# Performance work log

Measured on AMD Instinct MI355X. Metric: run time of the kernel, lower is better.

The kernel has to match this reference:

```python
import jax, jax.numpy as jnp
import numpy as np

B = 32          # graphs per batch
NPG = 512       # nodes per graph
EPG = 2048      # original edges per graph (stored in y[:, -1])
N = B * NPG     # 16384 nodes
E = B * EPG     # 65536 edges
GF = 5          # num_global_features
ETOT = E + N    # edges after add_self_loops

def _lin(k, o, i):
    return jax.random.normal(k, (o, i), jnp.float32) / np.sqrt(i)

def setup_inputs():
    key = jax.random.key(0)
    ks = jax.random.split(key, 20)
    x = jax.random.normal(ks[0], (N,), jnp.float32)
    off = (jnp.arange(B, dtype=jnp.int32) * NPG)[:, None]
    src = (jax.random.randint(ks[1], (B, EPG), 0, NPG, dtype=jnp.int32) + off).reshape(-1)
    dst = (jax.random.randint(ks[2], (B, EPG), 0, NPG, dtype=jnp.int32) + off).reshape(-1)
    edge_index = jnp.stack([src, dst])
    edge_attr = jax.random.normal(ks[3], (E, GF), jnp.float32)
    # last global feature = number of edges per graph (module reads y[:, -1])
    y = jax.random.normal(ks[4], (B, GF), jnp.float32).at[:, -1].set(float(EPG)).reshape(-1)
    batch_vector = jnp.repeat(jnp.arange(B, dtype=jnp.int32), NPG)
    p = dict(
        Wn=_lin(ks[5], 512, 1), bn=jnp.zeros(512, jnp.float32),
        We=_lin(ks[6], 511, GF), be=jnp.zeros(511, jnp.float32),
        Wg=_lin(ks[7], 512, GF), bg=jnp.zeros(512, jnp.float32),
        Wl=_lin(ks[8], 1024, 512), bl=jnp.zeros(1024, jnp.float32),
        Wr=_lin(ks[9], 1024, 512), br=jnp.zeros(1024, jnp.float32),
        Wge=_lin(ks[10], 1024, 511),
        att=jax.random.normal(ks[11], (1024,), jnp.float32) / 32.0,
        bgat=jnp.zeros(1024, jnp.float32),
        Wm=_lin(ks[12], 1024, 1024), bm=jnp.zeros(1024, jnp.float32),
        Wmi=_lin(ks[13], 1024, 1024), bmi=jnp.zeros(1024, jnp.float32),
        Wce=_lin(ks[14], 1024, 512), bce=jnp.zeros(1024, jnp.float32),
        W1=_lin(ks[15], 256, 2048), b1=jnp.zeros(256, jnp.float32),
        W2=_lin(ks[16], 1, 256), b2=jnp.zeros(1, jnp.float32),
    )
    return dict(x=x, edge_index=edge_index, edge_attr=edge_attr, y=y,
                batch_vector=batch_vector, **p)

def _leaky(v, s=0.01):
    return jnp.where(v >= 0, v, s * v)

def _forward(edge_index, batch_vector, x, edge_attr, y, Wn, bn, We, be, Wg, bg,
             Wl, bl, Wr, br, Wge, att, bgat, Wm, bm, Wmi, bmi, Wce, bce,
             W1, b1, W2, b2):
    # add_self_loops (fill_value=1.0 for edge_attr), self loops appended last
    loops = jnp.arange(N, dtype=edge_index.dtype)
    src = jnp.concatenate([edge_index[0], loops])
    dst = jnp.concatenate([edge_index[1], loops])
    ea = jnp.concatenate([edge_attr, jnp.ones((N, GF), edge_attr.dtype)], axis=0)
    # preprocessing MLPs (dropout = identity at inference)
    h = _leaky(x[:, None] @ Wn.T + bn)               # [N, 512]
    e = _leaky(ea @ We.T + be)                       # [ETOT, 511]
    yg = _leaky(y.reshape(B, GF) @ Wg.T + bg)        # [B, 512]
    # GATv2Conv, 1 head, concat, negative_slope=0.2, no self-loop add
    xl = h @ Wl.T + bl                               # source transform [N, 1024]
    xr = h @ Wr.T + br                               # target transform [N, 1024]
    m = _leaky(xl[src] + xr[dst] + e @ Wge.T, 0.2)   # [ETOT, 1024]
    logit = m @ att                                  # [ETOT]
    mx = jax.ops.segment_max(logit, dst, num_segments=N)
    ex = jnp.exp(logit - mx[dst])
    alpha = ex / (jax.ops.segment_sum(ex, dst, num_segments=N)[dst] + 1e-16)
    gat = jax.ops.segment_sum(alpha[:, None] * xl[src], dst, num_segments=N) + bgat
    edge_total = jnp.concatenate([e, alpha[:, None]], axis=1)  # [ETOT, 512]
    # GeneralConv: undirected message, add aggregation, identity skip (in==out)
    hm = gat @ Wm.T + bm
    hmi = gat @ Wmi.T + bmi
    eh = edge_total @ Wce.T + bce                    # [ETOT, 1024]
    deg = jax.ops.segment_sum(jnp.ones((ETOT,), gat.dtype), dst, num_segments=N)
    conv = (jax.ops.segment_sum(hm[src] + eh, dst, num_segments=N)
            + deg[:, None] * hmi + gat)              # [N, 1024]
    # global mean pooling (nodes) and module's contiguous edge batch vector
    nc = jax.ops.segment_sum(jnp.ones((N,), conv.dtype), batch_vector, num_segments=B)
    pn = jax.ops.segment_sum(conv, batch_vector, num_segments=B) / nc[:, None]
    ebatch = jnp.repeat(jnp.arange(B, dtype=jnp.int32), EPG + NPG)
    pe = jax.ops.segment_sum(edge_total, ebatch, num_segments=B) / float(EPG + NPG)
    pooled = jnp.concatenate([pn, pe, yg], axis=1)   # [B, 2048]
    out = _leaky(pooled @ W1.T + b1) @ W2.T + b2
    return jax.nn.sigmoid(out)                       # [B, 1]

def reference(x, edge_index, edge_attr, y, batch_vector, Wn, bn, We, be, Wg, bg,
              Wl, bl, Wr, br, Wge, att, bgat, Wm, bm, Wmi, bmi, Wce, bce,
              W1, b1, W2, b2):
    return _forward(edge_index, batch_vector, x, edge_attr, y, Wn, bn, We, be,
                    Wg, bg, Wl, bl, Wr, br, Wge, att, bgat, Wm, bm, Wmi, bmi,
                    Wce, bce, W1, b1, W2, b2)
```

## Files before the change

### kernel.cpp

```cpp
#include <hip/hip_runtime.h>
#include <cstdint>
#include <cstddef>

#define N_NODES 16384
#define N_EDGES 65536
#define ETOT    81920
#define B_GR    32

typedef __attribute__((ext_vector_type(8))) short bf16x8;
typedef __attribute__((ext_vector_type(4))) float f32x4;

static constexpr size_t OFF_XL    = 0;
static constexpr size_t OFF_XR    = 33554432ULL;
static constexpr size_t OFF_EBF   = 67108864ULL;
static constexpr size_t OFF_HBF   = 67108864ULL;
static constexpr size_t OFF_WCAT  = 83886080ULL;
static constexpr size_t OFF_ROWP  = 67108864ULL;
static constexpr size_t OFF_CSR   = 67174656ULL;
static constexpr size_t OFF_ALPHA = 67502336ULL;
static constexpr size_t OFF_WGEP  = 134217728ULL;
static constexpr size_t OFF_LPART = 135266304ULL;
static constexpr size_t OFF_DEG   = 137363456ULL;
static constexpr size_t OFF_ODEG  = 137428992ULL;
static constexpr size_t OFF_CURS  = 137494528ULL;
static constexpr size_t OFF_PG    = 137560064ULL;
static constexpr size_t OFF_PDG   = 137691136ULL;
static constexpr size_t OFF_PGAT  = 137822208ULL;
static constexpr size_t OFF_PS    = 137953280ULL;
static constexpr size_t OFF_PE    = 138018816ULL;
static constexpr size_t OFF_WLOOP = 138084352ULL;
static constexpr size_t OFF_YG    = 138088448ULL;
static constexpr size_t OFF_PN    = 138153984ULL;
static constexpr size_t OFF_OPRE  = 138285056ULL;

__device__ __forceinline__ float leaky01(float v){ return v >= 0.f ? v : 0.01f*v; }
__device__ __forceinline__ float leaky02(float v){ return v >= 0.f ? v : 0.2f*v; }
__device__ __forceinline__ unsigned short f2bf(float f){
  union { float f; unsigned u; } v; v.f = f;
  unsigned r = v.u + 0x7FFFu + ((v.u >> 16) & 1u);
  return (unsigned short)(r >> 16);
}
__device__ __forceinline__ float bf2f(unsigned short h){
  union { unsigned u; float f; } v; v.u = ((unsigned)h) << 16;
  return v.f;
}

__global__ __launch_bounds__(256) void k_prep0(
    const float* __restrict__ x, const float* __restrict__ Wn, const float* __restrict__ bn,
    const float* __restrict__ Wl, const float* __restrict__ Wr,
    const float* __restrict__ Wge, const float* __restrict__ y,
    const float* __restrict__ Wg, const float* __restrict__ bg,
    const float* __restrict__ We, const float* __restrict__ be,
    float* __restrict__ zone, unsigned short* __restrict__ h_bf,
    unsigned short* __restrict__ Wcat, unsigned short* __restrict__ Wge_p,
    float* __restrict__ yg, float* __restrict__ we_loop) {
  __shared__ float e_lds[512];
  int bx = blockIdx.x, tid = threadIdx.x;
  if (bx < 176) {
    ((float4*)zone)[bx*256 + tid] = (float4){0.f,0.f,0.f,0.f};
  } else if (bx < 1200) {
    int gid = (bx-176)*256 + tid;
    int base = gid*8;
    int n = base >> 9, j = base & 511;
    float xv = x[n];
    float4 w0 = *(const float4*)(Wn + j);
    float4 w1 = *(const float4*)(Wn + j + 4);
    float4 b0 = *(const float4*)(bn + j);
    float4 b1 = *(const float4*)(bn + j + 4);
    unsigned short o[8];
    o[0]=f2bf(leaky01(xv*w0.x+b0.x)); o[1]=f2bf(leaky01(xv*w0.y+b0.y));
    o[2]=f2bf(leaky01(xv*w0.z+b0.z)); o[3]=f2bf(leaky01(xv*w0.w+b0.w));
    o[4]=f2bf(leaky01(xv*w1.x+b1.x)); o[5]=f2bf(leaky01(xv*w1.y+b1.y));
    o[6]=f2bf(leaky01(xv*w1.z+b1.z)); o[7]=f2bf(leaky01(xv*w1.w+b1.w));
    ((uint4*)h_bf)[gid] = *(const uint4*)o;
  } else if (bx < 2224) {
    int i = (bx-1200)*256 + tid;
    int base = i*4;
    const float* src = (base < 524288) ? (Wl + base) : (Wr + base - 524288);
    float4 v = *(const float4*)src;
    ushort4 o; o.x=f2bf(v.x); o.y=f2bf(v.y); o.z=f2bf(v.z); o.w=f2bf(v.w);
    ((ushort4*)Wcat)[i] = o;
  } else if (bx < 4272) {
    int gid = (bx-2224)*256 + tid;
    int j = gid >> 9, k = gid & 511;
    Wge_p[gid] = (k < 511) ? f2bf(Wge[(size_t)j*511 + k]) : (unsigned short)0;
  } else if (bx < 4336) {
    int gid = (bx-4272)*256 + tid;
    int b = gid >> 9, j = gid & 511;
    float s = bg[j];
    #pragma unroll
    for (int k=0;k<5;k++) s += y[b*5+k]*Wg[j*5+k];
    yg[gid] = leaky01(s);
  } else {
    for (int c = tid; c < 512; c += 256) {
      float v = 0.f;
      if (c < 511) {
        float s = be[c];
        #pragma unroll
        for (int q=0;q<5;q++) s += We[c*5+q];
        v = leaky01(s);
      }
      e_lds[c] = v;
    }
    __syncthreads();
    int j = (bx-4336)*256 + tid;
    float s = 0.f;
    for (int k=0;k<511;k++) s += e_lds[k]*Wge[(size_t)j*511+k];
    we_loop[j] = s;
  }
}

__global__ __launch_bounds__(256) void k_prep_e(
    const float* __restrict__ ea, const float* __restrict__ We, const float* __restrict__ be,
    unsigned short* __restrict__ E_bf,
    const int* __restrict__ ei, int* __restrict__ deg, int* __restrict__ odeg) {
  int blk = blockIdx.x;
  if (blk < 16384) {
    int gid = blk*256 + threadIdx.x;
    int e = gid >> 6, cg = gid & 63;
    int c0 = cg*8;
    const float* e5 = ea + (size_t)e*5;
    float a0=e5[0], a1=e5[1], a2=e5[2], a3=e5[3], a4=e5[4];
    unsigned short o[8];
    #pragma unroll
    for (int j=0;j<8;j++) {
      int c = c0 + j;
      float v = 0.f;
      if (c < 511) {
        const float* w = We + c*5;
        float s = be[c] + a0*w[0] + a1*w[1] + a2*w[2] + a3*w[3] + a4*w[4];
        v = leaky01(s);
      }
      o[j] = f2bf(v);
    }
    ((uint4*)E_bf)[gid] = *(const uint4*)o;
  } else {
    int i = (blk-16384)*256 + threadIdx.x;
    int s, d;
    if (i < N_EDGES) { s = ei[i]; d = ei[N_EDGES + i]; }
    else { s = i - N_EDGES; d = s; }
    atomicAdd(&deg[d], 1);
    atomicAdd(&odeg[s], 1);
  }
}

__global__ __launch_bounds__(1024) void k_scan(const int* __restrict__ deg, int* __restrict__ rowptr) {
  __shared__ int sums[1024];
  int t = threadIdx.x;
  int local[16]; int s = 0;
  #pragma unroll
  for (int i=0;i<16;i++){ local[i] = deg[t*16+i]; s += local[i]; }
  sums[t] = s; __syncthreads();
  for (int off=1; off<1024; off<<=1) {
    int v = (t >= off) ? sums[t-off] : 0;
    __syncthreads();
    sums[t] += v;
    __syncthreads();
  }
  int run = (t==0) ? 0 : sums[t-1];
  if (t==0) rowptr[0] = 0;
  #pragma unroll
  for (int i=0;i<16;i++){ run += local[i]; rowptr[t*16+i+1] = run; }
}

__global__ void k_fill_csr(const int* __restrict__ ei, const int* __restrict__ rowptr,
                           int* __restrict__ cursor, int* __restrict__ csr) {
  int i = blockIdx.x*blockDim.x + threadIdx.x;
  int d = (i < N_EDGES) ? ei[N_EDGES + i] : (i - N_EDGES);
  int pos = rowptr[d] + atomicAdd(&cursor[d], 1);
  csr[pos] = i;
}


__global__ __launch_bounds__(256) void k_gemm_xlxr(
    const unsigned short* __restrict__ h_bf, const unsigned short* __restrict__ Wcat,
    const float* __restrict__ bl, const float* __restrict__ br,
    unsigned short* __restrict__ xl_bf, unsigned short* __restrict__ xr_bf) {
  __shared__ unsigned short As[2][4096];
  __shared__ unsigned short Bs[2][4096];
  int blk = blockIdx.x;
  int xcd = blk & 7, slot = blk >> 3;
  int bx = xcd*16 + (slot >> 4), by = slot & 15;
  int row0 = bx*128, col0 = by*128;
  int tid = threadIdx.x;
  int w = tid >> 6, lane = tid & 63;
  int wm = w >> 1, wn = w & 1;
  int quad = lane >> 4, l16 = lane & 15;
  int ldoff = w*512 + lane*8;
  const unsigned short* gA = h_bf + (size_t)(row0 + w*16 + l16)*512 + quad*8;
  const unsigned short* gB = Wcat + (size_t)(col0 + w*16 + l16)*512 + quad*8;
  f32x4 acc[4][4];
  #pragma unroll
  for (int i=0;i<4;i++)
    #pragma unroll
    for (int j=0;j<4;j++) acc[i][j] = (f32x4){0.f,0.f,0.f,0.f};

  {
    uint4 a0 = *(const uint4*)(gA);
    uint4 a1 = *(const uint4*)(gA + 32768);
    uint4 b0 = *(const uint4*)(gB);
    uint4 b1 = *(const uint4*)(gB + 32768);
    *(uint4*)&As[0][ldoff] = a0; *(uint4*)&As[0][2048+ldoff] = a1;
    *(uint4*)&Bs[0][ldoff] = b0; *(uint4*)&Bs[0][2048+ldoff] = b1;
  }
  __syncthreads();
  int cur = 0;
  #pragma unroll 2
  for (int k0 = 32; k0 <= 512; k0 += 32) {
    uint4 na0, na1, nb0, nb1;
    bool more = (k0 < 512);
    if (more) {
      na0 = *(const uint4*)(gA + k0);
      na1 = *(const uint4*)(gA + 32768 + k0);
      nb0 = *(const uint4*)(gB + k0);
      nb1 = *(const uint4*)(gB + 32768 + k0);
    }
    bf16x8 af[4], bfr[4];
    #pragma unroll
    for (int mi=0;mi<4;mi++)
      af[mi] = *(const bf16x8*)&As[cur][(wm*4+mi)*512 + quad*128 + l16*8];
    #pragma unroll
    for (int ni=0;ni<4;ni++)
      bfr[ni] = *(const bf16x8*)&Bs[cur][(wn*4+ni)*512 + quad*128 + l16*8];
    #pragma unroll
    for (int mi=0;mi<4;mi++)
      #pragma unroll
      for (int ni=0;ni<4;ni++)
        acc[mi][ni] = __builtin_amdgcn_mfma_f32_16x16x32_bf16(af[mi], bfr[ni], acc[mi][ni], 0, 0, 0);
    if (more) {
      *(uint4*)&As[cur^1][ldoff] = na0; *(uint4*)&As[cur^1][2048+ldoff] = na1;
      *(uint4*)&Bs[cur^1][ldoff] = nb0; *(uint4*)&Bs[cur^1][2048+ldoff] = nb1;
    }
    __syncthreads();
    cur ^= 1;
  }
  bool isL = (by < 8);
  const float* bias = isL ? bl : br;
  unsigned short* O = isL ? xl_bf : xr_bf;
  int cb = isL ? col0 : (col0 - 1024);
  float bias4[4];
  #pragma unroll
  for (int ni=0;ni<4;ni++) bias4[ni] = bias[cb + wn*64 + ni*16 + l16];
  #pragma unroll
  for (int mi=0;mi<4;mi++)
    #pragma unroll
    for (int ni=0;ni<4;ni++) {
      int col = cb + wn*64 + ni*16 + l16;
      #pragma unroll
      for (int r=0;r<4;r++) {
        int row = row0 + wm*64 + mi*16 + quad*4 + r;
        O[(size_t)row*1024 + col] = f2bf(acc[mi][ni][r] + bias4[ni]);
      }
    }
}

__global__ __launch_bounds__(256) void k_mfma_we(
    const unsigned short* __restrict__ E_bf, const unsigned short* __restrict__ Wge_bf,
    const int* __restrict__ ei,
    const unsigned short* __restrict__ xl_bf, const unsigned short* __restrict__ xr_bf,
    const float* __restrict__ att, float* __restrict__ logit_part) {
  __shared__ unsigned short As[2][4096];
  __shared__ unsigned short Bs[2][4096];
  __shared__ float tmp[128];
  int blk = blockIdx.x;
  int xcd = blk & 7, slot = blk >> 3;
  int bx = xcd*64 + (slot >> 3), by = slot & 7;
  int row0 = bx*128, col0 = by*128;
  int tid = threadIdx.x;
  int w = tid >> 6, lane = tid & 63;
  int wm = w >> 1, wn = w & 1;
  int quad = lane >> 4, l16 = lane & 15;
  int ldoff = w*512 + lane*8;
  const unsigned short* gA = E_bf  + (size_t)(row0 + w*16 + l16)*512 + quad*8;
  const unsigned short* gB = Wge_bf + (size_t)(col0 + w*16 + l16)*512 + quad*8;
  f32x4 acc[4][4];
  #pragma unroll
  for (int i=0;i<4;i++)
    #pragma unroll
    for (int j=0;j<4;j++) acc[i][j] = (f32x4){0.f,0.f,0.f,0.f};

  {
    uint4 a0 = *(const uint4*)(gA);
    uint4 a1 = *(const uint4*)(gA + 32768);
    uint4 b0 = *(const uint4*)(gB);
    uint4 b1 = *(const uint4*)(gB + 32768);
    *(uint4*)&As[0][ldoff] = a0; *(uint4*)&As[0][2048+ldoff] = a1;
    *(uint4*)&Bs[0][ldoff] = b0; *(uint4*)&Bs[0][2048+ldoff] = b1;
  }
  __syncthreads();
  int cur = 0;
  #pragma unroll 2
  for (int k0 = 32; k0 <= 512; k0 += 32) {
    uint4 na0, na1, nb0, nb1;
    bool more = (k0 < 512);
    if (more) {
      na0 = *(const uint4*)(gA + k0);
      na1 = *(const uint4*)(gA + 32768 + k0);
      nb0 = *(const uint4*)(gB + k0);
      nb1 = *(const uint4*)(gB + 32768 + k0);
    }
    bf16x8 af[4], bfr[4];
    #pragma unroll
    for (int mi=0;mi<4;mi++)
      af[mi] = *(const bf16x8*)&As[cur][(wm*4+mi)*512 + quad*128 + l16*8];
    #pragma unroll
    for (int ni=0;ni<4;ni++)
      bfr[ni] = *(const bf16x8*)&Bs[cur][(wn*4+ni)*512 + quad*128 + l16*8];
    #pragma unroll
    for (int mi=0;mi<4;mi++)
      #pragma unroll
      for (int ni=0;ni<4;ni++)
        acc[mi][ni] = __builtin_amdgcn_mfma_f32_16x16x32_bf16(af[mi], bfr[ni], acc[mi][ni], 0, 0, 0);
    if (more) {
      *(uint4*)&As[cur^1][ldoff] = na0; *(uint4*)&As[cur^1][2048+ldoff] = na1;
      *(uint4*)&Bs[cur^1][ldoff] = nb0; *(uint4*)&Bs[cur^1][2048+ldoff] = nb1;
    }
    __syncthreads();
    cur ^= 1;
  }
  float att4[4];
  #pragma unroll
  for (int ni=0;ni<4;ni++) att4[ni] = att[col0 + wn*64 + ni*16 + l16];
  float pv[4][4];
  #pragma unroll
  for (int mi=0;mi<4;mi++) {
    #pragma unroll
    for (int r=0;r<4;r++) {
      int e = row0 + wm*64 + mi*16 + quad*4 + r;
      int s = ei[e], d = ei[N_EDGES + e];
      const unsigned short* xlr = xl_bf + (size_t)s*1024;
      const unsigned short* xrr = xr_bf + (size_t)d*1024;
      float p = 0.f;
      #pragma unroll
      for (int ni=0;ni<4;ni++) {
        int col = col0 + wn*64 + ni*16 + l16;
        float z = acc[mi][ni][r] + bf2f(xlr[col]) + bf2f(xrr[col]);
        z = leaky02(z);
        p += z*att4[ni];
      }
      p += __shfl_down(p, 8, 16);
      p += __shfl_down(p, 4, 16);
      p += __shfl_down(p, 2, 16);
      p += __shfl_down(p, 1, 16);
      pv[mi][r] = p;
    }
  }
  if (wn == 1 && l16 == 0) {
    #pragma unroll
    for (int mi=0;mi<4;mi++)
      #pragma unroll
      for (int r=0;r<4;r++)
        tmp[wm*64 + mi*16 + quad*4 + r] = pv[mi][r];
  }
  __syncthreads();
  if (wn == 0 && l16 == 0) {
    #pragma unroll
    for (int mi=0;mi<4;mi++)
      #pragma unroll
      for (int r=0;r<4;r++) {
        int le = wm*64 + mi*16 + quad*4 + r;
        logit_part[(size_t)(row0 + le)*8 + by] = pv[mi][r] + tmp[le];
      }
  }
}

__global__ __launch_bounds__(256) void k_softmax_gat(
    const int* __restrict__ ei, const int* __restrict__ rowptr, const int* __restrict__ csr,
    const float* __restrict__ logit_part,
    const unsigned short* __restrict__ xl_bf, const unsigned short* __restrict__ xr_bf,
    const float* __restrict__ we_loop, const float* __restrict__ att,
    const float* __restrict__ bgat,
    float* __restrict__ alpha, unsigned short* __restrict__ gat_bf) {
  int blk = blockIdx.x;
  int wid = threadIdx.x >> 6, lane = threadIdx.x & 63;
  int n = ((blk & 7) << 11) + ((blk >> 3) << 2) + wid;
  int c0 = lane*16;

  float sll;
  {
    const uint4* xp = (const uint4*)(xl_bf + (size_t)n*1024 + c0);
    const uint4* rp = (const uint4*)(xr_bf + (size_t)n*1024 + c0);
    uint4 xa0 = xp[0], xa1 = xp[1];
    uint4 xb0 = rp[0], xb1 = rp[1];
    const unsigned short* ua = (const unsigned short*)&xa0;
    const unsigned short* ub = (const unsigned short*)&xb0;
    const unsigned short* ua1 = (const unsigned short*)&xa1;
    const unsigned short* ub1 = (const unsigned short*)&xb1;
    float s = 0.f;
    #pragma unroll
    for (int j=0;j<8;j++) {
      float z = bf2f(ua[j]) + bf2f(ub[j]) + we_loop[c0+j];
      s += leaky02(z) * att[c0+j];
    }
    #pragma unroll
    for (int j=0;j<8;j++) {
      float z = bf2f(ua1[j]) + bf2f(ub1[j]) + we_loop[c0+8+j];
      s += leaky02(z) * att[c0+8+j];
    }
    #pragma unroll
    for (int m=1; m<64; m<<=1) s += __shfl_xor(s, m);
    sll = s;
  }

  int beg = rowptr[n], end = rowptr[n+1];
  int cnt = end - beg;

  float acc[16];
  {
    const float4* bp = (const float4*)(bgat + c0);
    float4 b0 = bp[0], b1 = bp[1], b2 = bp[2], b3 = bp[3];
    acc[0]=b0.x; acc[1]=b0.y; acc[2]=b0.z; acc[3]=b0.w;
    acc[4]=b1.x; acc[5]=b1.y; acc[6]=b1.z; acc[7]=b1.w;
    acc[8]=b2.x; acc[9]=b2.y; acc[10]=b2.z; acc[11]=b2.w;
    acc[12]=b3.x; acc[13]=b3.y; acc[14]=b3.z; acc[15]=b3.w;
  }

  if (cnt <= 64) {
    int p = beg + lane;
    bool act = (p < end);
    int e = 0, src = 0;
    float lg = -1e30f;
    if (act) {
      e = csr[p];
      if (e < N_EDGES) {
        const float4* lp = (const float4*)(logit_part + (size_t)e*8);
        float4 q0 = lp[0], q1 = lp[1];
        lg = q0.x+q0.y+q0.z+q0.w+q1.x+q1.y+q1.z+q1.w;
        src = ei[e];
      } else { lg = sll; src = e - N_EDGES; }
    }
    float mx = lg;
    #pragma unroll
    for (int m=1; m<64; m<<=1) mx = fmaxf(mx, __shfl_xor(mx, m));
    float ex = act ? expf(lg - mx) : 0.f;
    float ss = ex;
    #pragma unroll
    for (int m=1; m<64; m<<=1) ss += __shfl_xor(ss, m);
    float a = ex * (1.f/(ss + 1e-16f));
    if (act) alpha[e] = a;
    for (int q = 0; q < cnt; q++) {
      float aq = __shfl(a, q);
      int sq = __shfl(src, q);
      const uint4* xp = (const uint4*)(xl_bf + (size_t)sq*1024 + c0);
      uint4 u0 = xp[0], u1 = xp[1];
      const unsigned short* uu0 = (const unsigned short*)&u0;
      const unsigned short* uu1 = (const unsigned short*)&u1;
      #pragma unroll
      for (int j=0;j<8;j++) acc[j]   += aq * bf2f(uu0[j]);
      #pragma unroll
      for (int j=0;j<8;j++) acc[8+j] += aq * bf2f(uu1[j]);
    }
  } else {
    float mx = -1e30f;
    for (int p = beg + lane; p < end; p += 64) {
      int e = csr[p];
      float lg;
      if (e < N_EDGES) {
        const float4* lp = (const float4*)(logit_part + (size_t)e*8);
        float4 q0 = lp[0], q1 = lp[1];
        lg = q0.x+q0.y+q0.z+q0.w+q1.x+q1.y+q1.z+q1.w;
      } else lg = sll;
      mx = fmaxf(mx, lg);
    }
    #pragma unroll
    for (int m=1; m<64; m<<=1) mx = fmaxf(mx, __shfl_xor(mx, m));
    float ss = 0.f;
    for (int p = beg + lane; p < end; p += 64) {
      int e = csr[p];
      float lg;
      if (e < N_EDGES) {
        const float4* lp = (const float4*)(logit_part + (size_t)e*8);
        float4 q0 = lp[0], q1 = lp[1];
        lg = q0.x+q0.y+q0.z+q0.w+q1.x+q1.y+q1.z+q1.w;
      } else lg = sll;
      ss += expf(lg - mx);
    }
    #pragma unroll
    for (int m=1; m<64; m<<=1) ss += __shfl_xor(ss, m);
    float inv = 1.f/(ss + 1e-16f);

    for (int p0 = beg; p0 < end; p0 += 64) {
      int p = p0 + lane;
      float a = 0.f; int src = 0;
      if (p < end) {
        int e = csr[p];
        float lg;
        if (e < N_EDGES) {
          const float4* lp = (const float4*)(logit_part + (size_t)e*8);
          float4 q0 = lp[0], q1 = lp[1];
          lg = q0.x+q0.y+q0.z+q0.w+q1.x+q1.y+q1.z+q1.w;
          src = ei[e];
        } else { lg = sll; src = e - N_EDGES; }
        a = expf(lg - mx)*inv;
        alpha[e] = a;
      }
      int kmax = end - p0; if (kmax > 64) kmax = 64;
      for (int q = 0; q < kmax; q++) {
        float aq = __shfl(a, q);
        int sq = __shfl(src, q);
        const uint4* xp = (const uint4*)(xl_bf + (size_t)sq*1024 + c0);
        uint4 u0 = xp[0], u1 = xp[1];
        const unsigned short* uu0 = (const unsigned short*)&u0;
        const unsigned short* uu1 = (const unsigned short*)&u1;
        #pragma unroll
        for (int j=0;j<8;j++) acc[j]   += aq * bf2f(uu0[j]);
        #pragma unroll
        for (int j=0;j<8;j++) acc[8+j] += aq * bf2f(uu1[j]);
      }
    }
  }

  unsigned short o[16];
  #pragma unroll
  for (int j=0;j<16;j++) o[j] = f2bf(acc[j]);
  uint4* gp = (uint4*)(gat_bf + (size_t)n*1024 + c0);
  gp[0] = *(const uint4*)&o[0];
  gp[1] = *(const uint4*)&o[8];
}

__global__ __launch_bounds__(256) void k_pool(
    const unsigned short* __restrict__ gat_bf, const int* __restrict__ odeg,
    const int* __restrict__ rowptr,
    float* __restrict__ P_G, float* __restrict__ P_DG, float* __restrict__ P_gat,
    const float* __restrict__ ea, const float* __restrict__ We, const float* __restrict__ be,
    const float* __restrict__ alpha, float* __restrict__ P_S, float* __restrict__ pe) {
  __shared__ float sea[640];
  __shared__ float sal[128];
  int slot = blockIdx.x, tid = threadIdx.x;
  if (slot < 512) {
    int b = slot >> 4, nc = slot & 15;
    int c4 = tid;
    float a1[4]={0,0,0,0}, a2[4]={0,0,0,0}, a3[4]={0,0,0,0};
    int n0 = b*512 + nc*32;
    for (int i=0;i<32;i++){
      int n = n0 + i;
      ushort4 g4 = ((const ushort4*)(gat_bf + (size_t)n*1024))[c4];
      float od = (float)odeg[n];
      float dg = (float)(rowptr[n+1]-rowptr[n]);
      float g0 = bf2f(g4.x), g1 = bf2f(g4.y), g2 = bf2f(g4.z), g3 = bf2f(g4.w);
      a1[0]+=od*g0; a1[1]+=od*g1; a1[2]+=od*g2; a1[3]+=od*g3;
      a2[0]+=dg*g0; a2[1]+=dg*g1; a2[2]+=dg*g2; a2[3]+=dg*g3;
      a3[0]+=g0; a3[1]+=g1; a3[2]+=g2; a3[3]+=g3;
    }
    #pragma unroll
    for (int j=0;j<4;j++){
      atomicAdd(&P_G [b*1024 + c4*4+j], a1[j]);
      atomicAdd(&P_DG[b*1024 + c4*4+j], a2[j]);
      atomicAdd(&P_gat[b*1024 + c4*4+j], a3[j]);
    }
  } else {
    int s = slot - 512;
    int b = s & 31, chy = s >> 5;
    int mode = (chy < 20) ? 0 : 1;
    int ch = (chy < 20) ? chy : (chy - 20);
    int c1 = tid, c2 = tid + 256;
    bool v2 = (c2 < 511);
    float w1[5], w2[5]={0,0,0,0,0}, b1v, b2v=0.f;
    #pragma unroll
    for (int q=0;q<5;q++) w1[q] = We[c1*5+q];
    b1v = be[c1];
    if (v2) {
      #pragma unroll
      for (int q=0;q<5;q++) w2[q] = We[c2*5+q];
      b2v = be[c2];
    }
    int base = (mode == 0)
      ? ((ch < 16) ? (b*2048 + ch*128) : (N_EDGES + b*512 + (ch-16)*128))
      : (b*2560 + ch*128);
    for (int i=tid;i<640;i+=256){
      int r = base + i/5;
      sea[i] = (r < N_EDGES) ? ea[(size_t)r*5 + (i%5)] : 1.0f;
    }
    for (int i=tid;i<128;i+=256) sal[i] = alpha[base + i];
    __syncthreads();
    float acc1 = 0.f, acc2 = 0.f;
    for (int rr=0; rr<128; rr++) {
      const float* er = &sea[rr*5];
      acc1 += leaky01(b1v + er[0]*w1[0]+er[1]*w1[1]+er[2]*w1[2]+er[3]*w1[3]+er[4]*w1[4]);
      if (v2) acc2 += leaky01(b2v + er[0]*w2[0]+er[1]*w2[1]+er[2]*w2[2]+er[3]*w2[3]+er[4]*w2[4]);
      else    acc2 += sal[rr];
    }
    if (mode == 0) {
      atomicAdd(&P_S[b*512+c1], acc1);
      atomicAdd(&P_S[b*512+c2], acc2);
    } else {
      const float sc = 1.f/2560.f;
      atomicAdd(&pe[b*512+c1], acc1*sc);
      atomicAdd(&pe[b*512+c2], acc2*sc);
    }
  }
}

__global__ __launch_bounds__(256) void k_pn(
    const float* __restrict__ P_G, const float* __restrict__ P_DG,
    const float* __restrict__ P_S, const float* __restrict__ P_gat,
    const float* __restrict__ Wm, const float* __restrict__ bm,
    const float* __restrict__ Wmi, const float* __restrict__ bmi,
    const float* __restrict__ Wce, const float* __restrict__ bce,
    float* __restrict__ pn, float* __restrict__ out_pre) {
  __shared__ float sPg[1024], sPdg[1024], sPs[512];
  int blk = blockIdx.x;
  int xcd = blk & 7, slot = blk >> 3;
  int colgrp = xcd*2 + (slot & 1);
  int b = slot >> 1;
  int col0 = colgrp*64;
  int tid = threadIdx.x, w = tid >> 6, lane = tid & 63;
  if (blk == 0 && tid < 32) out_pre[tid] = 0.f;
  for (int i=tid;i<1024;i+=256){ sPg[i]=P_G[b*1024+i]; sPdg[i]=P_DG[b*1024+i]; }
  for (int i=tid;i<512;i+=256) sPs[i]=P_S[b*512+i];
  __syncthreads();
  for (int c=0;c<16;c++){
    int j = col0 + w*16 + c;
    const float* wm  = Wm  + (size_t)j*1024;
    const float* wmi = Wmi + (size_t)j*1024;
    const float* wce = Wce + (size_t)j*512;
    float s = 0.f;
    #pragma unroll 4
    for (int i=0;i<16;i++){ int k = lane + i*64; s += sPg[k]*wm[k] + sPdg[k]*wmi[k]; }
    #pragma unroll 4
    for (int i=0;i<8;i++){ int k = lane + i*64; s += sPs[k]*wce[k]; }
    #pragma unroll
    for (int off=32; off; off>>=1) s += __shfl_down(s, off);
    if (lane == 0) {
      pn[b*1024+j] = (s + P_gat[b*1024+j] + 2560.f*(bm[j]+bmi[j]+bce[j])) * (1.f/512.f);
    }
  }
}

__global__ __launch_bounds__(256) void k_final(
    const float* __restrict__ pn, const float* __restrict__ pe, const float* __restrict__ yg,
    const float* __restrict__ W1, const float* __restrict__ b1,
    const float* __restrict__ W2, float* __restrict__ out_pre) {
  __shared__ float pooled[2048];
  int blk = blockIdx.x;
  int hc = blk & 7, b = blk >> 3;
  int tid = threadIdx.x;
  for (int i=tid;i<1024;i+=256) pooled[i]      = pn[b*1024+i];
  for (int i=tid;i<512;i+=256)  pooled[1024+i] = pe[b*512+i];
  for (int i=tid;i<512;i+=256)  pooled[1536+i] = yg[b*512+i];
  __syncthreads();
  int r = hc*32 + (tid >> 3);
  int seg = tid & 7;
  const float4* w4 = (const float4*)(W1 + (size_t)r*2048 + seg*256);
  const float4* p4 = (const float4*)(pooled + seg*256);
  float s = 0.f;
  #pragma unroll 8
  for (int k=0;k<64;k++){
    float4 w = w4[k]; float4 p = p4[k];
    s += w.x*p.x + w.y*p.y + w.z*p.z + w.w*p.w;
  }
  s += __shfl_down(s, 4, 8);
  s += __shfl_down(s, 2, 8);
  s += __shfl_down(s, 1, 8);
  if (seg == 0) {
    float h = leaky01(s + b1[r]);
    atomicAdd(&out_pre[b], h * W2[r]);
  }
}

__global__ void k_sigmoid(const float* __restrict__ out_pre, const float* __restrict__ b2,
                          float* __restrict__ out) {
  int b = threadIdx.x;
  out[b] = 1.f/(1.f + expf(-(out_pre[b] + b2[0])));
}

extern "C" void kernel_launch(void* const* d_in, const int* in_sizes, int n_in,
                              void* d_out, int out_size, void* d_ws, size_t ws_size,
                              hipStream_t stream) {
  const float* x   = (const float*)d_in[0];
  const int*   ei  = (const int*)  d_in[1];
  const float* ea  = (const float*)d_in[2];
  const float* y   = (const float*)d_in[3];
  const float* Wn  = (const float*)d_in[5];
  const float* bn  = (const float*)d_in[6];
  const float* We  = (const float*)d_in[7];
  const float* be  = (const float*)d_in[8];
  const float* Wg  = (const float*)d_in[9];
  const float* bg  = (const float*)d_in[10];
  const float* Wl  = (const float*)d_in[11];
  const float* bl  = (const float*)d_in[12];
  const float* Wr  = (const float*)d_in[13];
  const float* br  = (const float*)d_in[14];
  const float* Wge = (const float*)d_in[15];
  const float* att = (const float*)d_in[16];
  const float* bgat= (const float*)d_in[17];
  const float* Wm  = (const float*)d_in[18];
  const float* bm  = (const float*)d_in[19];
  const float* Wmi = (const float*)d_in[20];
  const float* bmi = (const float*)d_in[21];
  const float* Wce = (const float*)d_in[22];
  const float* bce = (const float*)d_in[23];
  const float* W1  = (const float*)d_in[24];
  const float* b1  = (const float*)d_in[25];
  const float* W2  = (const float*)d_in[26];
  const float* b2  = (const float*)d_in[27];
  float* out = (float*)d_out;

  char* ws = (char*)d_ws;
  unsigned short* xl_bf  = (unsigned short*)(ws + OFF_XL);
  unsigned short* xr_bf  = (unsigned short*)(ws + OFF_XR);
  unsigned short* gat_bf = (unsigned short*)(ws + OFF_XR);
  unsigned short* E_bf   = (unsigned short*)(ws + OFF_EBF);
  unsigned short* h_bf   = (unsigned short*)(ws + OFF_HBF);
  unsigned short* Wcat   = (unsigned short*)(ws + OFF_WCAT);
  unsigned short* Wge_p  = (unsigned short*)(ws + OFF_WGEP);
  float* lpart  = (float*)(ws + OFF_LPART);
  float* zone   = (float*)(ws + OFF_DEG);
  int*   deg    = (int*)  (ws + OFF_DEG);
  int*   odeg   = (int*)  (ws + OFF_ODEG);
  int*   cursor = (int*)  (ws + OFF_CURS);
  float* P_G    = (float*)(ws + OFF_PG);
  float* P_DG   = (float*)(ws + OFF_PDG);
  float* P_gat  = (float*)(ws + OFF_PGAT);
  float* P_S    = (float*)(ws + OFF_PS);
  float* pe     = (float*)(ws + OFF_PE);
  int*   rowptr = (int*)  (ws + OFF_ROWP);
  int*   csr    = (int*)  (ws + OFF_CSR);
  float* alpha  = (float*)(ws + OFF_ALPHA);
  float* we_loop= (float*)(ws + OFF_WLOOP);
  float* yg     = (float*)(ws + OFF_YG);
  float* pn     = (float*)(ws + OFF_PN);
  float* out_pre= (float*)(ws + OFF_OPRE);

  k_prep0<<<dim3(4340), dim3(256), 0, stream>>>(x, Wn, bn, Wl, Wr, Wge, y, Wg, bg, We, be,
                                                zone, h_bf, Wcat, Wge_p, yg, we_loop);
  k_gemm_xlxr<<<dim3(2048), dim3(256), 0, stream>>>(h_bf, Wcat, bl, br, xl_bf, xr_bf);
  k_prep_e<<<dim3(16704), dim3(256), 0, stream>>>(ea, We, be, E_bf, ei, deg, odeg);
  k_mfma_we<<<dim3(4096), dim3(256), 0, stream>>>(E_bf, Wge_p, ei, xl_bf, xr_bf, att, lpart);
  k_scan<<<dim3(1), dim3(1024), 0, stream>>>(deg, rowptr);
  k_fill_csr<<<dim3(320), dim3(256), 0, stream>>>(ei, rowptr, cursor, csr);
  k_softmax_gat<<<dim3(4096), dim3(256), 0, stream>>>(ei, rowptr, csr, lpart, xl_bf, xr_bf,
                                                      we_loop, att, bgat, alpha, gat_bf);
  k_pool<<<dim3(1792), dim3(256), 0, stream>>>(gat_bf, odeg, rowptr, P_G, P_DG, P_gat,
                                               ea, We, be, alpha, P_S, pe);
  k_pn<<<dim3(512), dim3(256), 0, stream>>>(P_G, P_DG, P_S, P_gat, Wm, bm, Wmi, bmi, Wce, bce,
                                            pn, out_pre);
  k_final<<<dim3(256), dim3(256), 0, stream>>>(pn, pe, yg, W1, b1, W2, out_pre);
  k_sigmoid<<<dim3(1), dim3(32), 0, stream>>>(out_pre, b2, out);
}
```

Before: 552.7 us.

## Replace node-feature GEMM with piecewise-linear prefix-sum tables over sorted breakpoints

The node embedding h = leaky(x*Wn+bn) comes from a scalar per node, so h@Wl^T and h@Wr^T are piecewise-linear in x. The change sorts the 512 breakpoints -bn/Wn, builds prefix-sum tables of Wl/Wr against Wn and bn, and evaluates each node with two binary searches plus table lookups. This removes the bf16 conversion of h and the weights and the MFMA GEMM. In exchange it adds a single-block sort and a table-build kernel that runs only 8 blocks, each thread serially walking 512 gathered weight entries. It also changes the rounding path, since the sums are now fp32 prefix sums instead of bf16 products.

```diff
diff --git a/kernel.cpp b/kernel.cpp
--- a/kernel.cpp
+++ b/kernel.cpp
@@ -13,8 +13,9 @@
 static constexpr size_t OFF_XL    = 0;
 static constexpr size_t OFF_XR    = 33554432ULL;
 static constexpr size_t OFF_EBF   = 67108864ULL;
-static constexpr size_t OFF_HBF   = 67108864ULL;
-static constexpr size_t OFF_WCAT  = 83886080ULL;
+static constexpr size_t OFF_SORT  = 67108864ULL;
+static constexpr size_t OFF_TAB   = 67125248ULL;
+static constexpr size_t TABSZ     = 513ULL*2048ULL*4ULL;
 static constexpr size_t OFF_ROWP  = 67108864ULL;
 static constexpr size_t OFF_CSR   = 67174656ULL;
 static constexpr size_t OFF_ALPHA = 67502336ULL;
@@ -46,46 +47,21 @@
 }
 
 __global__ __launch_bounds__(256) void k_prep0(
-    const float* __restrict__ x, const float* __restrict__ Wn, const float* __restrict__ bn,
-    const float* __restrict__ Wl, const float* __restrict__ Wr,
     const float* __restrict__ Wge, const float* __restrict__ y,
     const float* __restrict__ Wg, const float* __restrict__ bg,
     const float* __restrict__ We, const float* __restrict__ be,
-    float* __restrict__ zone, unsigned short* __restrict__ h_bf,
-    unsigned short* __restrict__ Wcat, unsigned short* __restrict__ Wge_p,
+    float* __restrict__ zone, unsigned short* __restrict__ Wge_p,
     float* __restrict__ yg, float* __restrict__ we_loop) {
   __shared__ float e_lds[512];
   int bx = blockIdx.x, tid = threadIdx.x;
   if (bx < 176) {
     ((float4*)zone)[bx*256 + tid] = (float4){0.f,0.f,0.f,0.f};
-  } else if (bx < 1200) {
+  } else if (bx < 2224) {
     int gid = (bx-176)*256 + tid;
-    int base = gid*8;
-    int n = base >> 9, j = base & 511;
-    float xv = x[n];
-    float4 w0 = *(const float4*)(Wn + j);
-    float4 w1 = *(const float4*)(Wn + j + 4);
-    float4 b0 = *(const float4*)(bn + j);
-    float4 b1 = *(const float4*)(bn + j + 4);
-    unsigned short o[8];
-    o[0]=f2bf(leaky01(xv*w0.x+b0.x)); o[1]=f2bf(leaky01(xv*w0.y+b0.y));
-    o[2]=f2bf(leaky01(xv*w0.z+b0.z)); o[3]=f2bf(leaky01(xv*w0.w+b0.w));
-    o[4]=f2bf(leaky01(xv*w1.x+b1.x)); o[5]=f2bf(leaky01(xv*w1.y+b1.y));
-    o[6]=f2bf(leaky01(xv*w1.z+b1.z)); o[7]=f2bf(leaky01(xv*w1.w+b1.w));
-    ((uint4*)h_bf)[gid] = *(const uint4*)o;
-  } else if (bx < 2224) {
-    int i = (bx-1200)*256 + tid;
-    int base = i*4;
-    const float* src = (base < 524288) ? (Wl + base) : (Wr + base - 524288);
-    float4 v = *(const float4*)src;
-    ushort4 o; o.x=f2bf(v.x); o.y=f2bf(v.y); o.z=f2bf(v.z); o.w=f2bf(v.w);
-    ((ushort4*)Wcat)[i] = o;
-  } else if (bx < 4272) {
-    int gid = (bx-2224)*256 + tid;
     int j = gid >> 9, k = gid & 511;
     Wge_p[gid] = (k < 511) ? f2bf(Wge[(size_t)j*511 + k]) : (unsigned short)0;
-  } else if (bx < 4336) {
-    int gid = (bx-4272)*256 + tid;
+  } else if (bx < 2288) {
+    int gid = (bx-2224)*256 + tid;
     int b = gid >> 9, j = gid & 511;
     float s = bg[j];
     #pragma unroll
@@ -103,10 +79,138 @@
       e_lds[c] = v;
     }
     __syncthreads();
-    int j = (bx-4336)*256 + tid;
+    int j = (bx-2288)*256 + tid;
     float s = 0.f;
     for (int k=0;k<511;k++) s += e_lds[k]*Wge[(size_t)j*511+k];
     we_loop[j] = s;
+  }
+}
+
+
+__global__ __launch_bounds__(512) void k_sort(
+    const float* __restrict__ Wn, const float* __restrict__ bn,
+    float* __restrict__ sTpos, float* __restrict__ sTneg,
+    int* __restrict__ posIdx, int* __restrict__ negIdx, int* __restrict__ meta) {
+  __shared__ float tS[512];
+  __shared__ int gS[512];
+  __shared__ int zflag;
+  int k = threadIdx.x;
+  if (k == 0) zflag = 0;
+  __syncthreads();
+  float wn = Wn[k], bk = bn[k];
+  const float INF = __builtin_inff();
+  int gp; float t;
+  if (wn > 0.f)      { gp = 1; t = -bk/wn; }
+  else if (wn < 0.f) { gp = 0; t = -bk/wn; }
+  else               { gp = 1; t = (bk >= 0.f) ? -INF : INF; }
+  tS[k] = t; gS[k] = gp;
+  if (bk != 0.f) atomicOr(&zflag, 1);
+  __syncthreads();
+  int rank = 0, cntP = 0;
+  for (int m = 0; m < 512; m++) {
+    cntP += gS[m];
+    if (gS[m] == gp) {
+      float tm = tS[m];
+      bool lt = gp ? (tm < t) : (tm > t);
+      if (lt || (tm == t && m < k)) rank++;
+    }
+  }
+  int cntN = 512 - cntP;
+  if (gp) { sTpos[rank] = t; posIdx[rank] = k; }
+  else    { sTneg[rank] = t; negIdx[rank] = k; }
+  if (k >= cntP) { sTpos[k] = INF;  posIdx[k] = 0; }
+  if (k >= cntN) { sTneg[k] = -INF; negIdx[k] = 0; }
+  if (k == 0) { meta[0] = cntP; meta[1] = cntN; meta[2] = (zflag == 0) ? 1 : 0; }
+}
+
+__global__ __launch_bounds__(256) void k_tab(
+    const float* __restrict__ Wn, const float* __restrict__ bn,
+    const float* __restrict__ Wl, const float* __restrict__ Wr,
+    const int* __restrict__ posIdx, const int* __restrict__ negIdx,
+    const int* __restrict__ meta,
+    float* __restrict__ SAp, float* __restrict__ SAn,
+    float* __restrict__ SBp, float* __restrict__ SBn) {
+  __shared__ float wnS[512], bnS[512];
+  __shared__ int piS[512], niS[512];
+  int tid = threadIdx.x;
+  for (int i = tid; i < 512; i += 256) {
+    wnS[i] = Wn[i]; bnS[i] = bn[i]; piS[i] = posIdx[i]; niS[i] = negIdx[i];
+  }
+  __syncthreads();
+  int j = blockIdx.x*256 + tid;
+  const float* Wrow = (j < 1024) ? (Wl + (size_t)j*512) : (Wr + (size_t)(j-1024)*512);
+  int cntP = meta[0], cntN = meta[1];
+  float aP = 0.f, bP = 0.f, aN = 0.f, bN = 0.f;
+  SAp[j] = 0.f; SAn[j] = 0.f; SBp[j] = 0.f; SBn[j] = 0.f;
+  for (int r = 0; r < 512; r++) {
+    if (r < cntP) { int k = piS[r]; float w = Wrow[k]; aP += w*wnS[k]; bP += w*bnS[k]; }
+    size_t o = (size_t)(r+1)*2048 + j;
+    SAp[o] = aP; SBp[o] = bP;
+    if (r < cntN) { int k = niS[r]; float w = Wrow[k]; aN += w*wnS[k]; bN += w*bnS[k]; }
+    SAn[o] = aN; SBn[o] = bN;
+  }
+}
+
+__global__ __launch_bounds__(256) void k_xlxr(
+    const float* __restrict__ x,
+    const float* __restrict__ sTpos, const float* __restrict__ sTneg,
+    const int* __restrict__ meta,
+    const float* __restrict__ SAp, const float* __restrict__ SAn,
+    const float* __restrict__ SBp, const float* __restrict__ SBn,
+    const float* __restrict__ bl, const float* __restrict__ br,
+    unsigned short* __restrict__ xl_bf, unsigned short* __restrict__ xr_bf) {
+  __shared__ float totA[2048], totB[2048];
+  __shared__ float xS[8];
+  __shared__ int rpS[8], rnS[8];
+  int tid = threadIdx.x, bid = blockIdx.x;
+  int cntP = meta[0], cntN = meta[1], bnzero = meta[2];
+  for (int i = tid; i < 2048; i += 256) {
+    totA[i] = 0.01f*(SAp[(size_t)cntP*2048 + i] + SAn[(size_t)cntN*2048 + i]);
+    totB[i] = bnzero ? 0.f : 0.01f*(SBp[(size_t)cntP*2048 + i] + SBn[(size_t)cntN*2048 + i]);
+  }
+  if (tid < 8) {
+    int n = bid*8 + tid;
+    float xv = x[n];
+    xS[tid] = xv;
+    int lo = 0, hi = 512;
+    while (lo < hi) { int mid = (lo+hi)>>1; if (sTpos[mid] <= xv) lo = mid+1; else hi = mid; }
+    rpS[tid] = lo;
+    lo = 0; hi = 512;
+    while (lo < hi) { int mid = (lo+hi)>>1; if (sTneg[mid] >= xv) lo = mid+1; else hi = mid; }
+    rnS[tid] = lo;
+  }
+  __syncthreads();
+  int j0 = tid*8;
+  bool isL = (j0 < 1024);
+  const float* bias = isL ? (bl + j0) : (br + (j0 - 1024));
+  float4 bb0 = *(const float4*)(bias);
+  float4 bb1 = *(const float4*)(bias + 4);
+  float bv[8] = {bb0.x,bb0.y,bb0.z,bb0.w,bb1.x,bb1.y,bb1.z,bb1.w};
+  unsigned short* O = isL ? xl_bf : xr_bf;
+  int jc = j0 & 1023;
+  for (int i = 0; i < 8; i++) {
+    int n = bid*8 + i;
+    float xv = xS[i];
+    size_t rp = (size_t)rpS[i]*2048 + j0, rn = (size_t)rnS[i]*2048 + j0;
+    float4 a0 = *(const float4*)(SAp + rp); float4 a1 = *(const float4*)(SAp + rp + 4);
+    float4 c0 = *(const float4*)(SAn + rn); float4 c1 = *(const float4*)(SAn + rn + 4);
+    float pa[8] = {a0.x+c0.x, a0.y+c0.y, a0.z+c0.z, a0.w+c0.w,
+                   a1.x+c1.x, a1.y+c1.y, a1.z+c1.z, a1.w+c1.w};
+    float pb[8] = {0.f,0.f,0.f,0.f,0.f,0.f,0.f,0.f};
+    if (!bnzero) {
+      float4 d0 = *(const float4*)(SBp + rp); float4 d1 = *(const float4*)(SBp + rp + 4);
+      float4 e0 = *(const float4*)(SBn + rn); float4 e1 = *(const float4*)(SBn + rn + 4);
+      pb[0]=d0.x+e0.x; pb[1]=d0.y+e0.y; pb[2]=d0.z+e0.z; pb[3]=d0.w+e0.w;
+      pb[4]=d1.x+e1.x; pb[5]=d1.y+e1.y; pb[6]=d1.z+e1.z; pb[7]=d1.w+e1.w;
+    }
+    unsigned short o[8];
+    #pragma unroll
+    for (int q=0;q<8;q++) {
+      float cA = totA[j0+q] + 0.99f*pa[q];
+      float cB = totB[j0+q] + 0.99f*pb[q];
+      o[q] = f2bf(xv*cA + cB + bv[q]);
+    }
+    *(uint4*)(O + (size_t)n*1024 + jc) = *(const uint4*)o;
   }
 }
 
@@ -171,88 +275,6 @@
   csr[pos] = i;
 }
 
-
-__global__ __launch_bounds__(256) void k_gemm_xlxr(
-    const unsigned short* __restrict__ h_bf, const unsigned short* __restrict__ Wcat,
-    const float* __restrict__ bl, const float* __restrict__ br,
-    unsigned short* __restrict__ xl_bf, unsigned short* __restrict__ xr_bf) {
-  __shared__ unsigned short As[2][4096];
-  __shared__ unsigned short Bs[2][4096];
-  int blk = blockIdx.x;
-  int xcd = blk & 7, slot = blk >> 3;
-  int bx = xcd*16 + (slot >> 4), by = slot & 15;
-  int row0 = bx*128, col0 = by*128;
-  int tid = threadIdx.x;
-  int w = tid >> 6, lane = tid & 63;
-  int wm = w >> 1, wn = w & 1;
-  int quad = lane >> 4, l16 = lane & 15;
-  int ldoff = w*512 + lane*8;
-  const unsigned short* gA = h_bf + (size_t)(row0 + w*16 + l16)*512 + quad*8;
-  const unsigned short* gB = Wcat + (size_t)(col0 + w*16 + l16)*512 + quad*8;
-  f32x4 acc[4][4];
-  #pragma unroll
-  for (int i=0;i<4;i++)
-    #pragma unroll
-    for (int j=0;j<4;j++) acc[i][j] = (f32x4){0.f,0.f,0.f,0.f};
-
-  {
-    uint4 a0 = *(const uint4*)(gA);
-    uint4 a1 = *(const uint4*)(gA + 32768);
-    uint4 b0 = *(const uint4*)(gB);
-    uint4 b1 = *(const uint4*)(gB + 32768);
-    *(uint4*)&As[0][ldoff] = a0; *(uint4*)&As[0][2048+ldoff] = a1;
-    *(uint4*)&Bs[0][ldoff] = b0; *(uint4*)&Bs[0][2048+ldoff] = b1;
-  }
-  __syncthreads();
-  int cur = 0;
-  #pragma unroll 2
-  for (int k0 = 32; k0 <= 512; k0 += 32) {
-    uint4 na0, na1, nb0, nb1;
-    bool more = (k0 < 512);
-    if (more) {
-      na0 = *(const uint4*)(gA + k0);
-      na1 = *(const uint4*)(gA + 32768 + k0);
-      nb0 = *(const uint4*)(gB + k0);
-      nb1 = *(const uint4*)(gB + 32768 + k0);
-    }
-    bf16x8 af[4], bfr[4];
-    #pragma unroll
-    for (int mi=0;mi<4;mi++)
-      af[mi] = *(const bf16x8*)&As[cur][(wm*4+mi)*512 + quad*128 + l16*8];
-    #pragma unroll
-    for (int ni=0;ni<4;ni++)
-      bfr[ni] = *(const bf16x8*)&Bs[cur][(wn*4+ni)*512 + quad*128 + l16*8];
-    #pragma unroll
-    for (int mi=0;mi<4;mi++)
-      #pragma unroll
-      for (int ni=0;ni<4;ni++)
-        acc[mi][ni] = __builtin_amdgcn_mfma_f32_16x16x32_bf16(af[mi], bfr[ni], acc[mi][ni], 0, 0, 0);
-    if (more) {
-      *(uint4*)&As[cur^1][ldoff] = na0; *(uint4*)&As[cur^1][2048+ldoff] = na1;
-      *(uint4*)&Bs[cur^1][ldoff] = nb0; *(uint4*)&Bs[cur^1][2048+ldoff] = nb1;
-    }
-    __syncthreads();
-    cur ^= 1;
-  }
-  bool isL = (by < 8);
-  const float* bias = isL ? bl : br;
-  unsigned short* O = isL ? xl_bf : xr_bf;
-  int cb = isL ? col0 : (col0 - 1024);
-  float bias4[4];
-  #pragma unroll
-  for (int ni=0;ni<4;ni++) bias4[ni] = bias[cb + wn*64 + ni*16 + l16];
-  #pragma unroll
-  for (int mi=0;mi<4;mi++)
-    #pragma unroll
-    for (int ni=0;ni<4;ni++) {
-      int col = cb + wn*64 + ni*16 + l16;
-      #pragma unroll
-      for (int r=0;r<4;r++) {
-        int row = row0 + wm*64 + mi*16 + quad*4 + r;
-        O[(size_t)row*1024 + col] = f2bf(acc[mi][ni][r] + bias4[ni]);
-      }
-    }
-}
 
 __global__ __launch_bounds__(256) void k_mfma_we(
     const unsigned short* __restrict__ E_bf, const unsigned short* __restrict__ Wge_bf,
@@ -701,9 +723,16 @@
   unsigned short* xr_bf  = (unsigned short*)(ws + OFF_XR);
   unsigned short* gat_bf = (unsigned short*)(ws + OFF_XR);
   unsigned short* E_bf   = (unsigned short*)(ws + OFF_EBF);
-  unsigned short* h_bf   = (unsigned short*)(ws + OFF_HBF);
-  unsigned short* Wcat   = (unsigned short*)(ws + OFF_WCAT);
   unsigned short* Wge_p  = (unsigned short*)(ws + OFF_WGEP);
+  float* sTpos  = (float*)(ws + OFF_SORT);
+  float* sTneg  = (float*)(ws + OFF_SORT + 2048);
+  int*   posIdx = (int*)  (ws + OFF_SORT + 4096);
+  int*   negIdx = (int*)  (ws + OFF_SORT + 6144);
+  int*   meta   = (int*)  (ws + OFF_SORT + 8192);
+  float* SAp    = (float*)(ws + OFF_TAB);
+  float* SAn    = (float*)(ws + OFF_TAB + TABSZ);
+  float* SBp    = (float*)(ws + OFF_TAB + 2*TABSZ);
+  float* SBn    = (float*)(ws + OFF_TAB + 3*TABSZ);
   float* lpart  = (float*)(ws + OFF_LPART);
   float* zone   = (float*)(ws + OFF_DEG);
   int*   deg    = (int*)  (ws + OFF_DEG);
@@ -722,9 +751,13 @@
   float* pn     = (float*)(ws + OFF_PN);
   float* out_pre= (float*)(ws + OFF_OPRE);
 
-  k_prep0<<<dim3(4340), dim3(256), 0, stream>>>(x, Wn, bn, Wl, Wr, Wge, y, Wg, bg, We, be,
-                                                zone, h_bf, Wcat, Wge_p, yg, we_loop);
-  k_gemm_xlxr<<<dim3(2048), dim3(256), 0, stream>>>(h_bf, Wcat, bl, br, xl_bf, xr_bf);
+  k_prep0<<<dim3(2292), dim3(256), 0, stream>>>(Wge, y, Wg, bg, We, be,
+                                                zone, Wge_p, yg, we_loop);
+  k_sort<<<dim3(1), dim3(512), 0, stream>>>(Wn, bn, sTpos, sTneg, posIdx, negIdx, meta);
+  k_tab<<<dim3(8), dim3(256), 0, stream>>>(Wn, bn, Wl, Wr, posIdx, negIdx, meta,
+                                           SAp, SAn, SBp, SBn);
+  k_xlxr<<<dim3(2048), dim3(256), 0, stream>>>(x, sTpos, sTneg, meta, SAp, SAn, SBp, SBn,
+                                               bl, br, xl_bf, xr_bf);
   k_prep_e<<<dim3(16704), dim3(256), 0, stream>>>(ea, We, be, E_bf, ei, deg, odeg);
   k_mfma_we<<<dim3(4096), dim3(256), 0, stream>>>(E_bf, Wge_p, ei, xl_bf, xr_bf, att, lpart);
   k_scan<<<dim3(1), dim3(1024), 0, stream>>>(deg, rowptr);
```

Result: slower. 685.9 us (+24.1%).
